# Optimization experiments

Hardware: AMD Instinct MI355X
Metric: run time of the kernel (lower is better)

The kernel has to match this reference:

```python
import jax, jax.numpy as jnp
import numpy as np

TOKENS = 16384
HIDDEN = 2048
FFN = 8192


def setup_inputs() -> dict:
    key = jax.random.key(0)
    k_x, k_w1, k_w2 = jax.random.split(key, 3)
    x = jax.random.normal(k_x, (TOKENS, HIDDEN), dtype=jnp.float32)
    # PyTorch Linear default init scale ~ 1/sqrt(fan_in); use small scale for stability
    w1 = jax.random.normal(k_w1, (HIDDEN, FFN), dtype=jnp.float32) * (1.0 / np.sqrt(HIDDEN))
    b1 = jnp.zeros((FFN,), dtype=jnp.float32)
    w2 = jax.random.normal(k_w2, (FFN, HIDDEN), dtype=jnp.float32) * (1.0 / np.sqrt(FFN))
    b2 = jnp.zeros((HIDDEN,), dtype=jnp.float32)
    return {"x": x, "w1": w1, "b1": b1, "w2": w2, "b2": b2}


def reference(x, w1, b1, w2, b2):
    # all_to_all with equal split sizes on a single group is an identity
    # permutation of token chunks; on one device it is exactly identity.
    # dispatch (identity) -> MLP -> combine (identity)
    h = jax.nn.gelu(x @ w1 + b1, approximate=False)  # (tokens, ffn), exact erf GELU as torch nn.GELU
    y = h @ w2 + b2  # (tokens, hidden)
    return y
```

## Files before the change

### kernel.cpp

```cpp
#include <hip/hip_runtime.h>
#include <hip/hip_bf16.h>
#include <cstdint>
#include <cstddef>

typedef __bf16 bf16_t;
typedef __bf16 bf16x8 __attribute__((ext_vector_type(8)));
typedef float  f32x4  __attribute__((ext_vector_type(4)));

#define TOKENS 16384
#define HIDDEN 2048
#define FFN    8192

__device__ __forceinline__ void gload_lds16(const bf16_t* g, bf16_t* l) {
    __builtin_amdgcn_global_load_lds((const __attribute__((address_space(1))) void*)g,
                                     (__attribute__((address_space(3))) void*)l,
                                     16, 0, 0);
}

__global__ void cvt_f32_to_bf16(const float* __restrict__ in, bf16_t* __restrict__ out, int n8) {
    int i = blockIdx.x * blockDim.x + threadIdx.x;
    if (i >= n8) return;
    size_t base = (size_t)i * 8;
    f32x4 v0 = *(const f32x4*)&in[base];
    f32x4 v1 = *(const f32x4*)&in[base + 4];
    bf16x8 o;
    o[0] = (bf16_t)v0[0]; o[1] = (bf16_t)v0[1]; o[2] = (bf16_t)v0[2]; o[3] = (bf16_t)v0[3];
    o[4] = (bf16_t)v1[0]; o[5] = (bf16_t)v1[1]; o[6] = (bf16_t)v1[2]; o[7] = (bf16_t)v1[3];
    *(bf16x8*)&out[base] = o;
}

__global__ void transpose_cvt(const float* __restrict__ src, bf16_t* __restrict__ dst,
                              int R, int C) {
    __shared__ bf16_t tile[64][66];
    const int tcols = C >> 6;
    const int bx = blockIdx.x % tcols;
    const int by = blockIdx.x / tcols;
    const int c0 = bx << 6, r0 = by << 6;
    const int t = threadIdx.x;
#pragma unroll
    for (int i = 0; i < 16; ++i) {
        int idx = i * 256 + t;
        int rr = idx >> 6, cc = idx & 63;
        tile[rr][cc] = (bf16_t)src[(size_t)(r0 + rr) * C + (c0 + cc)];
    }
    __syncthreads();
#pragma unroll
    for (int i = 0; i < 16; ++i) {
        int idx = i * 256 + t;
        int cc = idx >> 6, rr = idx & 63;
        dst[(size_t)(c0 + cc) * R + (r0 + rr)] = tile[rr][cc];
    }
}

template<bool GELU_EPI, int M, int N, int K>
__global__ __launch_bounds__(256, 2)
void gemm_bt(const bf16_t* __restrict__ A,
             const bf16_t* __restrict__ BT,
             const float* __restrict__ bias,
             void* __restrict__ out)
{
    constexpr int BM = 128, BN = 128, BK = 64;
    __shared__ bf16_t As[BM * BK];
    __shared__ bf16_t Bs[BN * BK];

    const int t    = threadIdx.x;
    const int wave = t >> 6;
    const int lane = t & 63;
    const int bn = blockIdx.x % (N / BN);
    const int bm = blockIdx.x / (N / BN);

    const int wr = wave >> 1;
    const int wc = wave & 1;
    const int fr = lane & 15;
    const int fq = lane >> 4;

    f32x4 acc[4][4] = {};

    const int srow = wave * 8 + (lane >> 3);
    const int scol = (lane & 7) * 8;
    const bf16_t* gA = A  + (size_t)(bm * BM + srow) * K + scol;
    const bf16_t* gB = BT + (size_t)(bn * BN + srow) * K + scol;
    bf16_t* lA = &As[wave * 512];
    bf16_t* lB = &Bs[wave * 512];

    for (int kt = 0; kt < K / BK; ++kt) {
        const int k0 = kt * BK;
#pragma unroll
        for (int p = 0; p < 4; ++p) {
            gload_lds16(gA + (size_t)(p * 32) * K + k0, lA + p * 2048);
            gload_lds16(gB + (size_t)(p * 32) * K + k0, lB + p * 2048);
        }
        __syncthreads();
#pragma unroll
        for (int ks = 0; ks < 2; ++ks) {
            bf16x8 af[4], bfr[4];
#pragma unroll
            for (int i = 0; i < 4; ++i)
                af[i] = *(const bf16x8*)&As[(wr * 64 + i * 16 + fr) * BK + ks * 32 + fq * 8];
#pragma unroll
            for (int j = 0; j < 4; ++j)
                bfr[j] = *(const bf16x8*)&Bs[(wc * 64 + j * 16 + fr) * BK + ks * 32 + fq * 8];
#pragma unroll
            for (int i = 0; i < 4; ++i)
#pragma unroll
                for (int j = 0; j < 4; ++j)
                    acc[i][j] = __builtin_amdgcn_mfma_f32_16x16x32_bf16(af[i], bfr[j], acc[i][j], 0, 0, 0);
        }
        __syncthreads();
    }

    const int orow = bm * BM + wr * 64 + fq * 4;
    const int ocol = bn * BN + wc * 64 + fr;
#pragma unroll
    for (int i = 0; i < 4; ++i) {
#pragma unroll
        for (int j = 0; j < 4; ++j) {
            const int c = ocol + j * 16;
            const float bv = bias[c];
#pragma unroll
            for (int v = 0; v < 4; ++v) {
                const int r = orow + i * 16 + v;
                float xv = acc[i][j][v] + bv;
                if constexpr (GELU_EPI) {
                    float g = 0.5f * xv * (1.0f + erff(xv * 0.70710678118654752f));
                    ((bf16_t*)out)[(size_t)r * N + c] = (bf16_t)g;
                } else {
                    ((float*)out)[(size_t)r * N + c] = xv;
                }
            }
        }
    }
}

extern "C" void kernel_launch(void* const* d_in, const int* in_sizes, int n_in,
                              void* d_out, int out_size, void* d_ws, size_t ws_size,
                              hipStream_t stream) {
    const float* x  = (const float*)d_in[0];
    const float* w1 = (const float*)d_in[1];
    const float* b1 = (const float*)d_in[2];
    const float* w2 = (const float*)d_in[3];
    const float* b2 = (const float*)d_in[4];
    float* y = (float*)d_out;

    const size_t xb_elems  = (size_t)TOKENS * HIDDEN;
    const size_t w1t_elems = (size_t)FFN * HIDDEN;
    const size_t w2t_elems = (size_t)HIDDEN * FFN;
    const size_t h_elems   = (size_t)TOKENS * FFN;
    const size_t need = (xb_elems + w1t_elems + w2t_elems + h_elems) * sizeof(bf16_t);
    if (ws_size < need) return;

    char* ws = (char*)d_ws;
    bf16_t* xb  = (bf16_t*)ws;
    bf16_t* w1t = xb + xb_elems;
    bf16_t* w2t = w1t + w1t_elems;
    bf16_t* h   = w2t + w2t_elems;

    cvt_f32_to_bf16<<<(TOKENS * HIDDEN / 8 + 255) / 256, 256, 0, stream>>>(
        x, xb, TOKENS * HIDDEN / 8);
    transpose_cvt<<<(HIDDEN / 64) * (FFN / 64), 256, 0, stream>>>(w1, w1t, HIDDEN, FFN);
    transpose_cvt<<<(FFN / 64) * (HIDDEN / 64), 256, 0, stream>>>(w2, w2t, FFN, HIDDEN);
    gemm_bt<true, TOKENS, FFN, HIDDEN>
        <<<(TOKENS / 128) * (FFN / 128), 256, 0, stream>>>(xb, w1t, b1, h);
    gemm_bt<false, TOKENS, HIDDEN, FFN>
        <<<(TOKENS / 128) * (HIDDEN / 128), 256, 0, stream>>>(h, w2t, b2, y);
}
```

Before: 1.312 ms.

## Replace GEMM with 256x256 8-wave double-buffered pipelined kernel with swizzled LDS

Replaces the simple 128x128 single-buffered GEMM with a 256x256-tile, 512-thread kernel. The new kernel double-buffers LDS, interleaves async global-to-LDS loads with quarter-tile MFMA batches, raises wave priority around MFMAs, XOR-swizzles the LDS layout to avoid bank conflicts, and remaps workgroup IDs for cache locality. The aim is to hide memory latency and raise MFMA utilisation in both GEMMs. The cost is 128KB of LDS per block and a heavy barrier schedule, which may limit occupancy.

```diff
diff --git a/kernel.cpp b/kernel.cpp
--- a/kernel.cpp
+++ b/kernel.cpp
@@ -52,75 +52,180 @@
     }
 }
 
+#define BAR() __builtin_amdgcn_s_barrier()
+#define LGKM0() do { asm volatile("s_waitcnt lgkmcnt(0)" ::: "memory"); \
+                     __builtin_amdgcn_sched_barrier(0); } while (0)
+#define VMW(n) asm volatile("s_waitcnt vmcnt(" #n ")" ::: "memory")
+#define PRIO1() __builtin_amdgcn_s_setprio(1)
+#define PRIO0() __builtin_amdgcn_s_setprio(0)
+
+#define DS_A(BUF, QM) do { \
+    _Pragma("unroll") for (int mf = 0; mf < 4; ++mf) \
+    _Pragma("unroll") for (int ks = 0; ks < 2; ++ks) \
+        af[mf][ks] = *(const bf16x8*)&smem[(BUF)*16384 + wr*8192 + (((QM)*4+mf)*2+ks)*512 + lnb_e]; \
+} while (0)
+
+#define DS_B(BUF, QN, BB) do { \
+    _Pragma("unroll") for (int nf = 0; nf < 2; ++nf) \
+    _Pragma("unroll") for (int ks = 0; ks < 2; ++ks) \
+        BB[nf][ks] = *(const bf16x8*)&smem[32768 + (BUF)*16384 + bhalf + (((QN)*2+nf)*2+ks)*512 + lnb_e]; \
+} while (0)
+
+#define MFMA_Q(QM, QN, BB) do { \
+    _Pragma("unroll") for (int ks = 0; ks < 2; ++ks) \
+    _Pragma("unroll") for (int mf = 0; mf < 4; ++mf) \
+    _Pragma("unroll") for (int nf = 0; nf < 2; ++nf) \
+        acc[(QM)*4+mf][(QN)*2+nf] = __builtin_amdgcn_mfma_f32_16x16x32_bf16( \
+            af[mf][ks], BB[nf][ks], acc[(QM)*4+mf][(QN)*2+nf], 0, 0, 0); \
+} while (0)
+
+#define STAGE(GBASE, HROWS, TILE, EOFF) do { \
+    gload_lds16((GBASE) + aoff0 + (size_t)(HROWS) * K + (TILE) * 64, \
+                &smem[(EOFF) + wave * 512]); \
+    gload_lds16((GBASE) + aoff1 + (size_t)(HROWS) * K + (TILE) * 64, \
+                &smem[(EOFF) + 4096 + wave * 512]); \
+} while (0)
+
 template<bool GELU_EPI, int M, int N, int K>
-__global__ __launch_bounds__(256, 2)
-void gemm_bt(const bf16_t* __restrict__ A,
-             const bf16_t* __restrict__ BT,
-             const float* __restrict__ bias,
-             void* __restrict__ out)
+__global__ __launch_bounds__(512, 2)
+void gemm8p(const bf16_t* __restrict__ A, const bf16_t* __restrict__ BT,
+            const float* __restrict__ bias, void* __restrict__ out)
 {
-    constexpr int BM = 128, BN = 128, BK = 64;
-    __shared__ bf16_t As[BM * BK];
-    __shared__ bf16_t Bs[BN * BK];
-
-    const int t    = threadIdx.x;
-    const int wave = t >> 6;
-    const int lane = t & 63;
-    const int bn = blockIdx.x % (N / BN);
-    const int bm = blockIdx.x / (N / BN);
-
-    const int wr = wave >> 1;
-    const int wc = wave & 1;
-    const int fr = lane & 15;
-    const int fq = lane >> 4;
-
-    f32x4 acc[4][4] = {};
-
-    const int srow = wave * 8 + (lane >> 3);
-    const int scol = (lane & 7) * 8;
-    const bf16_t* gA = A  + (size_t)(bm * BM + srow) * K + scol;
-    const bf16_t* gB = BT + (size_t)(bn * BN + srow) * K + scol;
-    bf16_t* lA = &As[wave * 512];
-    bf16_t* lB = &Bs[wave * 512];
-
-    for (int kt = 0; kt < K / BK; ++kt) {
-        const int k0 = kt * BK;
-#pragma unroll
-        for (int p = 0; p < 4; ++p) {
-            gload_lds16(gA + (size_t)(p * 32) * K + k0, lA + p * 2048);
-            gload_lds16(gB + (size_t)(p * 32) * K + k0, lB + p * 2048);
-        }
-        __syncthreads();
-#pragma unroll
-        for (int ks = 0; ks < 2; ++ks) {
-            bf16x8 af[4], bfr[4];
-#pragma unroll
-            for (int i = 0; i < 4; ++i)
-                af[i] = *(const bf16x8*)&As[(wr * 64 + i * 16 + fr) * BK + ks * 32 + fq * 8];
-#pragma unroll
-            for (int j = 0; j < 4; ++j)
-                bfr[j] = *(const bf16x8*)&Bs[(wc * 64 + j * 16 + fr) * BK + ks * 32 + fq * 8];
-#pragma unroll
-            for (int i = 0; i < 4; ++i)
-#pragma unroll
-                for (int j = 0; j < 4; ++j)
-                    acc[i][j] = __builtin_amdgcn_mfma_f32_16x16x32_bf16(af[i], bfr[j], acc[i][j], 0, 0, 0);
-        }
-        __syncthreads();
-    }
-
-    const int orow = bm * BM + wr * 64 + fq * 4;
-    const int ocol = bn * BN + wc * 64 + fr;
-#pragma unroll
-    for (int i = 0; i < 4; ++i) {
-#pragma unroll
-        for (int j = 0; j < 4; ++j) {
-            const int c = ocol + j * 16;
+    constexpr int BM = 256, BN = 256;
+    constexpr int NT = K / 64, NI = NT / 2;
+    constexpr int NBN = N / BN;
+    __shared__ __align__(128) bf16_t smem[65536];
+
+    const int t = threadIdx.x;
+    const int wave = t >> 6, lane = t & 63;
+    const int fr = lane & 15, fq = lane >> 4;
+    const int wr = wave >> 2, wc = wave & 3;
+
+    int wg = blockIdx.x;
+    { const int cpx = (int)gridDim.x >> 3; wg = (wg & 7) * cpx + (wg >> 3); }
+    const int bm = wg / NBN, bn = wg % NBN;
+    const int rowA0 = bm * BM, colB0 = bn * BN;
+
+    int sr0, sk0, sr1, sk1;
+    {
+        int o = t * 16;
+        int ri = (o >> 6) & 15;
+        int b = (o & 63) ^ ((ri & 8) << 2);
+        sr0 = ((o >> 10) >> 1) * 16 + ri;
+        sk0 = ((o >> 10) & 1) * 32 + (b >> 1);
+        o = 8192 + t * 16;
+        ri = (o >> 6) & 15;
+        b = (o & 63) ^ ((ri & 8) << 2);
+        sr1 = ((o >> 10) >> 1) * 16 + ri;
+        sk1 = ((o >> 10) & 1) * 32 + (b >> 1);
+    }
+    const bf16_t* gA0 = A + (size_t)rowA0 * K;
+    const bf16_t* gB0 = BT + (size_t)colB0 * K;
+    const size_t aoff0 = (size_t)sr0 * K + sk0;
+    const size_t aoff1 = (size_t)sr1 * K + sk1;
+
+    const int lnb_e = fr * 32 + ((fq * 8) ^ ((fr & 8) << 1));
+    const int bhalf = (wc >> 1) * 8192 + (wc & 1) * 4096;
+
+    f32x4 acc[8][4] = {};
+    bf16x8 af[4][2], b0[2][2], b1[2][2];
+
+    STAGE(gA0, 0,   0, 0);
+    STAGE(gA0, 128, 0, 8192);
+    STAGE(gB0, 0,   0, 32768);
+    STAGE(gB0, 128, 0, 40960);
+    STAGE(gA0, 0,   1, 16384);
+    STAGE(gB0, 0,   1, 49152);
+    STAGE(gB0, 128, 1, 57344);
+    VMW(6);
+    BAR();
+
+    for (int i = 0; i < NI - 1; ++i) {
+        const int t1 = 2 * i + 1, t2 = 2 * i + 2, t3 = 2 * i + 3;
+        DS_A(0, 0); DS_B(0, 0, b0);
+        STAGE(gA0, 128, t1, 24576);
+        BAR(); LGKM0();
+        PRIO1(); MFMA_Q(0, 0, b0); PRIO0();
+        BAR();
+        DS_B(0, 1, b1);
+        BAR(); LGKM0();
+        PRIO1(); MFMA_Q(0, 1, b1); PRIO0();
+        BAR();
+        DS_A(0, 1);
+        STAGE(gB0, 0, t2, 32768);
+        BAR(); LGKM0();
+        PRIO1(); MFMA_Q(1, 1, b1); PRIO0();
+        BAR();
+        STAGE(gB0, 128, t2, 40960);
+        STAGE(gA0, 0,   t2, 0);
+        VMW(6);
+        BAR();
+        PRIO1(); MFMA_Q(1, 0, b0); PRIO0();
+        BAR();
+        DS_A(1, 0); DS_B(1, 0, b0);
+        STAGE(gA0, 128, t2, 8192);
+        BAR(); LGKM0();
+        PRIO1(); MFMA_Q(0, 0, b0); PRIO0();
+        BAR();
+        DS_B(1, 1, b1);
+        BAR(); LGKM0();
+        PRIO1(); MFMA_Q(0, 1, b1); PRIO0();
+        BAR();
+        DS_A(1, 1);
+        STAGE(gB0, 0, t3, 49152);
+        BAR(); LGKM0();
+        PRIO1(); MFMA_Q(1, 1, b1); PRIO0();
+        BAR();
+        STAGE(gB0, 128, t3, 57344);
+        STAGE(gA0, 0,   t3, 16384);
+        VMW(6);
+        BAR();
+        PRIO1(); MFMA_Q(1, 0, b0); PRIO0();
+        BAR();
+    }
+
+    DS_A(0, 0); DS_B(0, 0, b0);
+    STAGE(gA0, 128, NT - 1, 24576);
+    BAR(); LGKM0();
+    PRIO1(); MFMA_Q(0, 0, b0); PRIO0();
+    BAR();
+    DS_B(0, 1, b1);
+    BAR(); LGKM0();
+    PRIO1(); MFMA_Q(0, 1, b1); PRIO0();
+    BAR();
+    DS_A(0, 1);
+    BAR(); LGKM0();
+    PRIO1(); MFMA_Q(1, 1, b1); PRIO0();
+    BAR();
+    VMW(0);
+    BAR();
+    PRIO1(); MFMA_Q(1, 0, b0); PRIO0();
+    BAR();
+    DS_A(1, 0); DS_B(1, 0, b0);
+    BAR(); LGKM0();
+    PRIO1(); MFMA_Q(0, 0, b0); PRIO0();
+    BAR();
+    DS_B(1, 1, b1);
+    BAR(); LGKM0();
+    PRIO1(); MFMA_Q(0, 1, b1); PRIO0();
+    BAR();
+    DS_A(1, 1);
+    BAR(); LGKM0();
+    PRIO1(); MFMA_Q(1, 1, b1); PRIO0();
+    MFMA_Q(1, 0, b0);
+
+    const int orow = rowA0 + wr * 128 + fq * 4;
+    const int ocol = colB0 + wc * 64 + fr;
+#pragma unroll
+    for (int mf = 0; mf < 8; ++mf) {
+#pragma unroll
+        for (int nf = 0; nf < 4; ++nf) {
+            const int c = ocol + nf * 16;
             const float bv = bias[c];
 #pragma unroll
             for (int v = 0; v < 4; ++v) {
-                const int r = orow + i * 16 + v;
-                float xv = acc[i][j][v] + bv;
+                const int r = orow + mf * 16 + v;
+                float xv = acc[mf][nf][v] + bv;
                 if constexpr (GELU_EPI) {
                     float g = 0.5f * xv * (1.0f + erff(xv * 0.70710678118654752f));
                     ((bf16_t*)out)[(size_t)r * N + c] = (bf16_t)g;
@@ -159,8 +264,9 @@
         x, xb, TOKENS * HIDDEN / 8);
     transpose_cvt<<<(HIDDEN / 64) * (FFN / 64), 256, 0, stream>>>(w1, w1t, HIDDEN, FFN);
     transpose_cvt<<<(FFN / 64) * (HIDDEN / 64), 256, 0, stream>>>(w2, w2t, FFN, HIDDEN);
-    gemm_bt<true, TOKENS, FFN, HIDDEN>
-        <<<(TOKENS / 128) * (FFN / 128), 256, 0, stream>>>(xb, w1t, b1, h);
-    gemm_bt<false, TOKENS, HIDDEN, FFN>
-        <<<(TOKENS / 128) * (HIDDEN / 128), 256, 0, stream>>>(h, w2t, b2, y);
-}
+
+    gemm8p<true, TOKENS, FFN, HIDDEN>
+        <<<(TOKENS / 256) * (FFN / 256), 512, 0, stream>>>(xb, w1t, b1, h);
+    gemm8p<false, TOKENS, HIDDEN, FFN>
+        <<<(TOKENS / 256) * (HIDDEN / 256), 512, 0, stream>>>(h, w2t, b2, y);
+}
```

New measurement: 1.102 ms. -16.0%, faster.
